# Performance work log

Hardware: AMD Instinct MI355X
Metric: run time of the kernel (lower is better)

Reference implementation:

```python
import jax, jax.numpy as jnp
import numpy as np


def setup_inputs() -> dict:
    key = jax.random.key(0)
    k1, k2 = jax.random.split(key)
    inputs = jax.random.normal(k1, (16, 64, 64, 512), dtype=jnp.float32)
    gamma = jax.random.normal(k2, (1,), dtype=jnp.float32)
    return {"inputs": inputs, "gamma": gamma}


def reference(inputs, gamma):
    # inputs: [B, H, W, C] (NHWC), gamma: [1]
    b, h, w, c = inputs.shape
    vec_a = inputs.reshape(b, h * w, c)           # [B, HW, C]
    # channel-channel Gram matrix: [B, C, C]
    aTa = jnp.einsum('bnc,bnd->bcd', vec_a, vec_a)
    softmax_aTa = jax.nn.softmax(aTa, axis=-1)     # softmax over last channel axis
    # attend over channels: [B, HW, C] @ [B, C, C] -> [B, HW, C]
    aaTa = jnp.einsum('bnc,bcd->bnd', vec_a, softmax_aTa)
    aaTa = aaTa.reshape(b, h, w, c)
    return gamma * aaTa + inputs
```

## Files before the change

kernel.cpp:

```cpp
#include <hip/hip_runtime.h>
#include <stdint.h>

#define BB 16
#define NN 4096
#define CC 512
#define PELEM ((size_t)BB * CC * CC)

typedef __attribute__((ext_vector_type(8))) short bf16x8;
typedef __attribute__((ext_vector_type(4))) float f32x4;

__device__ __forceinline__ unsigned short to_bf16(float f) {
  unsigned int u = __float_as_uint(f);
  u += 0x7fffu + ((u >> 16) & 1u);
  return (unsigned short)(u >> 16);
}
__device__ __forceinline__ float bf16_to_f32(unsigned short h) {
  return __uint_as_float(((unsigned int)h) << 16);
}

__device__ __forceinline__ void gload_lds16(const void* g, void* l) {
  __builtin_amdgcn_global_load_lds(
      (const __attribute__((address_space(1))) unsigned int*)g,
      (__attribute__((address_space(3))) unsigned int*)l, 16, 0, 0);
}

template <int RS, int KLEN>
__device__ __forceinline__ void nt_gemm(const unsigned short* __restrict__ aB,
                                        const unsigned short* __restrict__ bB,
                                        f32x4 acc[4][4],
                                        unsigned short* lds) {
  const int tid  = threadIdx.x;
  const int wid  = tid >> 6;
  const int lane = tid & 63;
  const int wr   = (wid >> 1) * 64;
  const int wc   = (wid & 1) * 64;

  const f32x4 zero = {0.f, 0.f, 0.f, 0.f};
#pragma unroll
  for (int i = 0; i < 4; ++i)
#pragma unroll
    for (int j = 0; j < 4; ++j) acc[i][j] = zero;

  const int srow = lane >> 3;
  const int gsrc = (lane & 7) ^ srow;
  constexpr int NT = KLEN / 64;

  auto stage = [&](int bf, int k0) {
#pragma unroll
    for (int i = 0; i < 4; ++i) {
      const int issue = wid * 4 + i;
      const int row   = issue * 8 + srow;
      const size_t go = (size_t)row * RS + k0 + gsrc * 8;
      gload_lds16(aB + go, lds + bf * 16384 + issue * 512);
      gload_lds16(bB + go, lds + bf * 16384 + 8192 + issue * 512);
    }
  };
  auto compute = [&](int bf) {
    const unsigned short* lA = lds + bf * 16384;
    const unsigned short* lB = lA + 8192;
#pragma unroll
    for (int s = 0; s < 2; ++s) {
      bf16x8 af[4], bfr[4];
#pragma unroll
      for (int mf = 0; mf < 4; ++mf) {
        const int row = wr + mf * 16 + (lane & 15);
        const int ch  = (s * 4 + (lane >> 4)) ^ (row & 7);
        af[mf] = *(const bf16x8*)(lA + row * 64 + ch * 8);
      }
#pragma unroll
      for (int nf = 0; nf < 4; ++nf) {
        const int row = wc + nf * 16 + (lane & 15);
        const int ch  = (s * 4 + (lane >> 4)) ^ (row & 7);
        bfr[nf] = *(const bf16x8*)(lB + row * 64 + ch * 8);
      }
#pragma unroll
      for (int mf = 0; mf < 4; ++mf)
#pragma unroll
        for (int nf = 0; nf < 4; ++nf)
          acc[mf][nf] = __builtin_amdgcn_mfma_f32_16x16x32_bf16(
              af[mf], bfr[nf], acc[mf][nf], 0, 0, 0);
    }
  };

  stage(0, 0);
  __syncthreads();
  int cur = 0;
#pragma unroll 1
  for (int t = 0; t < NT; ++t) {
    if (t + 1 < NT) stage(cur ^ 1, (t + 1) * 64);
    compute(cur);
    __syncthreads();
    cur ^= 1;
  }
}

__global__ __launch_bounds__(256) void k_convert(const float* __restrict__ in,
                                                 unsigned short* __restrict__ a16,
                                                 unsigned short* __restrict__ at16) {
  __shared__ unsigned short lt[64 * 68];
  const int b  = blockIdx.y;
  const int tn = blockIdx.x >> 3, tc = blockIdx.x & 7;
  const int n0 = tn * 64, c0 = tc * 64;
  const int t   = threadIdx.x;
  const int ctc = t & 15;
  const int ntq = t >> 4;

  const float* src = in + ((size_t)b * NN + n0 + 4 * ntq) * CC + c0 + 4 * ctc;
  unsigned short* adst = a16 + ((size_t)b * NN + n0 + 4 * ntq) * CC + c0 + 4 * ctc;

  unsigned short ob[4][4];
#pragma unroll
  for (int j = 0; j < 4; ++j) {
    float4 v = *(const float4*)(src + (size_t)j * CC);
    ob[j][0] = to_bf16(v.x); ob[j][1] = to_bf16(v.y);
    ob[j][2] = to_bf16(v.z); ob[j][3] = to_bf16(v.w);
    ushort4 o = {ob[j][0], ob[j][1], ob[j][2], ob[j][3]};
    *(ushort4*)(adst + (size_t)j * CC) = o;
  }
#pragma unroll
  for (int q = 0; q < 4; ++q) {
    ushort4 w = {ob[0][q], ob[1][q], ob[2][q], ob[3][q]};
    *(ushort4*)&lt[(4 * ctc + q) * 68 + 4 * ntq] = w;
  }
  __syncthreads();

  const int c_l = t >> 2, w4 = t & 3;
  const unsigned short* lr = lt + c_l * 68;
  uint2 r0a = *(const uint2*)(lr + 8 * w4);
  uint2 r0b = *(const uint2*)(lr + 8 * w4 + 4);
  uint2 r1a = *(const uint2*)(lr + 8 * w4 + 32);
  uint2 r1b = *(const uint2*)(lr + 8 * w4 + 36);
  unsigned short* tb = at16 + ((size_t)b * CC + c0 + c_l) * NN + n0;
  uint4 s0 = {r0a.x, r0a.y, r0b.x, r0b.y};
  uint4 s1 = {r1a.x, r1a.y, r1b.x, r1b.y};
  *(uint4*)(tb + 8 * w4)      = s0;
  *(uint4*)(tb + 8 * w4 + 32) = s1;
}

__global__ __launch_bounds__(256) void k_gram(const unsigned short* __restrict__ at,
                                              float* __restrict__ parts) {
  __shared__ __align__(16) unsigned short lds[32768];
  const int bid  = blockIdx.x;
  const int work = (bid & 7) * 80 + (bid >> 3);
  const int b    = work / 40;
  const int r    = work % 40;
  const int ks   = r / 10;
  const int t10  = r % 10;
  const int ti = t10 < 4 ? 0 : t10 < 7 ? 1 : t10 < 9 ? 2 : 3;
  const int tj = t10 < 4 ? t10 : t10 < 7 ? t10 - 3 : t10 < 9 ? t10 - 5 : 3;
  const int c0 = ti * 128, d0 = tj * 128;

  const unsigned short* aB = at + ((size_t)b * CC + c0) * NN + ks * 1024;
  const unsigned short* bB = at + ((size_t)b * CC + d0) * NN + ks * 1024;
  f32x4 acc[4][4];
  nt_gemm<NN, 1024>(aB, bB, acc, lds);

  const int tid = threadIdx.x;
  const int lane = tid & 63, wid = tid >> 6;
  const int wr = (wid >> 1) * 64, wc = (wid & 1) * 64;
  float* gb = parts + (size_t)ks * PELEM + (size_t)b * CC * CC;

#pragma unroll
  for (int mf = 0; mf < 4; ++mf)
#pragma unroll
    for (int nf = 0; nf < 4; ++nf)
#pragma unroll
      for (int q = 0; q < 4; ++q) {
        const int row = c0 + wr + mf * 16 + (lane >> 4) * 4 + q;
        const int col = d0 + wc + nf * 16 + (lane & 15);
        gb[(size_t)row * CC + col] = acc[mf][nf][q];
      }

  if (c0 != d0) {
    float* sf = (float*)lds;
#pragma unroll 1
    for (int h = 0; h < 2; ++h) {
      __syncthreads();
      if ((wid >> 1) == h) {
#pragma unroll
        for (int mf = 0; mf < 4; ++mf)
#pragma unroll
          for (int nf = 0; nf < 4; ++nf)
#pragma unroll
            for (int q = 0; q < 4; ++q) {
              const int row_l = mf * 16 + (lane >> 4) * 4 + q;
              const int col   = wc + nf * 16 + (lane & 15);
              sf[row_l * 132 + col] = acc[mf][nf][q];
            }
      }
      __syncthreads();
      const int d_l = tid >> 1;
      const int rh  = tid & 1;
      float vals[32];
#pragma unroll
      for (int u = 0; u < 32; ++u) vals[u] = sf[(32 * rh + u) * 132 + d_l];
      float* dst = gb + (size_t)(d0 + d_l) * CC + c0 + 64 * h + 32 * rh;
#pragma unroll
      for (int s = 0; s < 8; ++s) {
        float4 w = {vals[4 * s], vals[4 * s + 1], vals[4 * s + 2], vals[4 * s + 3]};
        *(float4*)(dst + 4 * s) = w;
      }
    }
  }
}

__global__ __launch_bounds__(256) void k_softmax(const float* __restrict__ parts,
                                                 unsigned short* __restrict__ st) {
  __shared__ unsigned short ls[32][512];
  const int b  = blockIdx.x >> 4;
  const int cb = blockIdx.x & 15;
  const int wid = threadIdx.x >> 6, lane = threadIdx.x & 63;

#pragma unroll 1
  for (int i = 0; i < 8; ++i) {
    const int rl = wid * 8 + i;
    const int c  = cb * 32 + rl;
    const int r7 = rl & 7;
    const float* base = parts + ((size_t)b * CC + c) * CC;
    float4 v0 = {0.f, 0.f, 0.f, 0.f}, v1 = {0.f, 0.f, 0.f, 0.f};
#pragma unroll
    for (int p = 0; p < 4; ++p) {
      float4 a = *(const float4*)(base + (size_t)p * PELEM + lane * 4);
      float4 bq = *(const float4*)(base + (size_t)p * PELEM + 256 + lane * 4);
      v0.x += a.x; v0.y += a.y; v0.z += a.z; v0.w += a.w;
      v1.x += bq.x; v1.y += bq.y; v1.z += bq.z; v1.w += bq.w;
    }
    float m = fmaxf(fmaxf(fmaxf(v0.x, v0.y), fmaxf(v0.z, v0.w)),
                    fmaxf(fmaxf(v1.x, v1.y), fmaxf(v1.z, v1.w)));
#pragma unroll
    for (int off = 32; off > 0; off >>= 1) m = fmaxf(m, __shfl_xor(m, off));
    float e0 = expf(v0.x - m), e1 = expf(v0.y - m), e2 = expf(v0.z - m), e3 = expf(v0.w - m);
    float e4 = expf(v1.x - m), e5 = expf(v1.y - m), e6 = expf(v1.z - m), e7 = expf(v1.w - m);
    float s = e0 + e1 + e2 + e3 + e4 + e5 + e6 + e7;
#pragma unroll
    for (int off = 32; off > 0; off >>= 1) s += __shfl_xor(s, off);
    const float pinv = 1.0f / s;
    ushort4 o0, o1;
    o0.x = to_bf16(e0 * pinv); o0.y = to_bf16(e1 * pinv);
    o0.z = to_bf16(e2 * pinv); o0.w = to_bf16(e3 * pinv);
    o1.x = to_bf16(e4 * pinv); o1.y = to_bf16(e5 * pinv);
    o1.z = to_bf16(e6 * pinv); o1.w = to_bf16(e7 * pinv);
    *(ushort4*)&ls[rl][(lane ^ r7) << 2]         = o0;
    *(ushort4*)&ls[rl][256 + ((lane ^ r7) << 2)] = o1;
  }
  __syncthreads();

#pragma unroll 1
  for (int i = 0; i < 2; ++i) {
    const int d = i * 256 + threadIdx.x;
    unsigned int u[16];
#pragma unroll
    for (int k = 0; k < 16; ++k) {
      const int c0i = 2 * k, c1i = 2 * k + 1;
      const unsigned int lo = ls[c0i][(((d >> 2) ^ (c0i & 7)) << 2) | (d & 3)];
      const unsigned int hi = ls[c1i][(((d >> 2) ^ (c1i & 7)) << 2) | (d & 3)];
      u[k] = lo | (hi << 16);
    }
    unsigned short* dst = st + ((size_t)b * CC + d) * CC + cb * 32;
    uint4 w0 = {u[0], u[1], u[2], u[3]};
    uint4 w1 = {u[4], u[5], u[6], u[7]};
    uint4 w2 = {u[8], u[9], u[10], u[11]};
    uint4 w3 = {u[12], u[13], u[14], u[15]};
    *(uint4*)(dst + 0)  = w0;
    *(uint4*)(dst + 8)  = w1;
    *(uint4*)(dst + 16) = w2;
    *(uint4*)(dst + 24) = w3;
  }
}

__global__ __launch_bounds__(256) void k_out(const unsigned short* __restrict__ a16,
                                             const unsigned short* __restrict__ st,
                                             const float* __restrict__ gammap,
                                             float* __restrict__ outp) {
  __shared__ __align__(16) unsigned short lds[32768];
  const int bid  = blockIdx.x;
  const int work = (bid & 7) * 256 + (bid >> 3);
  const int b    = work >> 7;
  const int r    = work & 127;
  const int nt   = r >> 5;
  const int mt   = r & 31;
  const int n0 = mt * 128, d0 = nt * 128;
  const unsigned short* aB = a16 + ((size_t)b * NN + n0) * CC;
  const unsigned short* bB = st + ((size_t)b * CC + d0) * CC;
  f32x4 acc[4][4];
  nt_gemm<CC, CC>(aB, bB, acc, lds);

  const float g = gammap[0];
  const int lane = threadIdx.x & 63, wid = threadIdx.x >> 6;
  const int wr = (wid >> 1) * 64, wc = (wid & 1) * 64;
  const unsigned short* xr = a16 + ((size_t)b * NN + n0) * CC + d0;
  float* ob = outp + ((size_t)b * NN + n0) * CC + d0;
#pragma unroll
  for (int mf = 0; mf < 4; ++mf)
#pragma unroll
    for (int nf = 0; nf < 4; ++nf)
#pragma unroll
      for (int q = 0; q < 4; ++q) {
        const int row = wr + mf * 16 + (lane >> 4) * 4 + q;
        const int col = wc + nf * 16 + (lane & 15);
        const size_t off = (size_t)row * CC + col;
        ob[off] = fmaf(g, acc[mf][nf][q], bf16_to_f32(xr[off]));
      }
}

extern "C" void kernel_launch(void* const* d_in, const int* in_sizes, int n_in,
                              void* d_out, int out_size, void* d_ws, size_t ws_size,
                              hipStream_t stream) {
  const float* in    = (const float*)d_in[0];
  const float* gamma = (const float*)d_in[1];
  float* outp = (float*)d_out;

  unsigned short* a16  = (unsigned short*)d_ws;
  unsigned short* stb  = (unsigned short*)((char*)d_ws + ((size_t)64 << 20));
  unsigned short* at16 = (unsigned short*)d_out;
  float*          parts = (float*)((char*)d_out + ((size_t)64 << 20));

  k_convert<<<dim3(512, 16), 256, 0, stream>>>(in, a16, at16);
  k_gram<<<dim3(640), 256, 0, stream>>>(at16, parts);
  k_softmax<<<dim3(256), 256, 0, stream>>>(parts, stb);
  k_out<<<dim3(2048), 256, 0, stream>>>(a16, stb, gamma, outp);
}
```

Before: 356.7 us.

## Enlarge GEMM tiles to 256x256 with 512-thread blocks; compute full Gram

The shared NT-GEMM routine moves from 128x128 tiles with 4 waves to 256x256 tiles with 8 waves. Each wave now holds an 8x4 grid of MFMA accumulators, and the double-buffered LDS staging area grows to 128 KB. The Gram kernel stops using symmetry: it computes all four 256x256 quadrants directly and drops the LDS transpose that mirrored the off-diagonal tiles. The aim is more data reuse per LDS load and fewer, larger blocks. The cost is extra Gram FLOPs, one block per CU with less latency hiding, and higher register pressure.

```diff
diff --git a/kernel.cpp b/kernel.cpp
--- a/kernel.cpp
+++ b/kernel.cpp
@@ -25,19 +25,19 @@
 }
 
 template <int RS, int KLEN>
-__device__ __forceinline__ void nt_gemm(const unsigned short* __restrict__ aB,
-                                        const unsigned short* __restrict__ bB,
-                                        f32x4 acc[4][4],
-                                        unsigned short* lds) {
+__device__ __forceinline__ void nt_gemm256(const unsigned short* __restrict__ aB,
+                                           const unsigned short* __restrict__ bB,
+                                           f32x4 acc[8][4],
+                                           unsigned short* lds) {
   const int tid  = threadIdx.x;
   const int wid  = tid >> 6;
   const int lane = tid & 63;
-  const int wr   = (wid >> 1) * 64;
-  const int wc   = (wid & 1) * 64;
+  const int wr   = (wid >> 2) * 128;
+  const int wc   = (wid & 3) * 64;
 
   const f32x4 zero = {0.f, 0.f, 0.f, 0.f};
 #pragma unroll
-  for (int i = 0; i < 4; ++i)
+  for (int i = 0; i < 8; ++i)
 #pragma unroll
     for (int j = 0; j < 4; ++j) acc[i][j] = zero;
 
@@ -51,18 +51,18 @@
       const int issue = wid * 4 + i;
       const int row   = issue * 8 + srow;
       const size_t go = (size_t)row * RS + k0 + gsrc * 8;
-      gload_lds16(aB + go, lds + bf * 16384 + issue * 512);
-      gload_lds16(bB + go, lds + bf * 16384 + 8192 + issue * 512);
+      gload_lds16(aB + go, lds + bf * 32768 + issue * 512);
+      gload_lds16(bB + go, lds + bf * 32768 + 16384 + issue * 512);
     }
   };
   auto compute = [&](int bf) {
-    const unsigned short* lA = lds + bf * 16384;
-    const unsigned short* lB = lA + 8192;
+    const unsigned short* lA = lds + bf * 32768;
+    const unsigned short* lB = lA + 16384;
 #pragma unroll
     for (int s = 0; s < 2; ++s) {
-      bf16x8 af[4], bfr[4];
-#pragma unroll
-      for (int mf = 0; mf < 4; ++mf) {
+      bf16x8 af[8], bfr[4];
+#pragma unroll
+      for (int mf = 0; mf < 8; ++mf) {
         const int row = wr + mf * 16 + (lane & 15);
         const int ch  = (s * 4 + (lane >> 4)) ^ (row & 7);
         af[mf] = *(const bf16x8*)(lA + row * 64 + ch * 8);
@@ -74,7 +74,7 @@
         bfr[nf] = *(const bf16x8*)(lB + row * 64 + ch * 8);
       }
 #pragma unroll
-      for (int mf = 0; mf < 4; ++mf)
+      for (int mf = 0; mf < 8; ++mf)
 #pragma unroll
         for (int nf = 0; nf < 4; ++nf)
           acc[mf][nf] = __builtin_amdgcn_mfma_f32_16x16x32_bf16(
@@ -137,31 +137,27 @@
   *(uint4*)(tb + 8 * w4 + 32) = s1;
 }
 
-__global__ __launch_bounds__(256) void k_gram(const unsigned short* __restrict__ at,
-                                              float* __restrict__ parts) {
-  __shared__ __align__(16) unsigned short lds[32768];
+__global__ __launch_bounds__(512, 1) void k_gram(const unsigned short* __restrict__ at,
+                                                 float* __restrict__ parts) {
+  __shared__ __align__(16) unsigned short lds[65536];
   const int bid  = blockIdx.x;
-  const int work = (bid & 7) * 80 + (bid >> 3);
-  const int b    = work / 40;
-  const int r    = work % 40;
-  const int ks   = r / 10;
-  const int t10  = r % 10;
-  const int ti = t10 < 4 ? 0 : t10 < 7 ? 1 : t10 < 9 ? 2 : 3;
-  const int tj = t10 < 4 ? t10 : t10 < 7 ? t10 - 3 : t10 < 9 ? t10 - 5 : 3;
-  const int c0 = ti * 128, d0 = tj * 128;
-
+  const int work = (bid & 7) * 32 + (bid >> 3);
+  const int b    = work >> 4;
+  const int r    = work & 15;
+  const int ks   = r >> 2;
+  const int tile = r & 3;
+  const int c0 = (tile & 1) * 256;
+  const int d0 = (tile >> 1) * 256;
   const unsigned short* aB = at + ((size_t)b * CC + c0) * NN + ks * 1024;
   const unsigned short* bB = at + ((size_t)b * CC + d0) * NN + ks * 1024;
-  f32x4 acc[4][4];
-  nt_gemm<NN, 1024>(aB, bB, acc, lds);
-
-  const int tid = threadIdx.x;
-  const int lane = tid & 63, wid = tid >> 6;
-  const int wr = (wid >> 1) * 64, wc = (wid & 1) * 64;
+  f32x4 acc[8][4];
+  nt_gemm256<NN, 1024>(aB, bB, acc, lds);
+
+  const int lane = threadIdx.x & 63, wid = threadIdx.x >> 6;
+  const int wr = (wid >> 2) * 128, wc = (wid & 3) * 64;
   float* gb = parts + (size_t)ks * PELEM + (size_t)b * CC * CC;
-
-#pragma unroll
-  for (int mf = 0; mf < 4; ++mf)
+#pragma unroll
+  for (int mf = 0; mf < 8; ++mf)
 #pragma unroll
     for (int nf = 0; nf < 4; ++nf)
 #pragma unroll
@@ -170,38 +166,6 @@
         const int col = d0 + wc + nf * 16 + (lane & 15);
         gb[(size_t)row * CC + col] = acc[mf][nf][q];
       }
-
-  if (c0 != d0) {
-    float* sf = (float*)lds;
-#pragma unroll 1
-    for (int h = 0; h < 2; ++h) {
-      __syncthreads();
-      if ((wid >> 1) == h) {
-#pragma unroll
-        for (int mf = 0; mf < 4; ++mf)
-#pragma unroll
-          for (int nf = 0; nf < 4; ++nf)
-#pragma unroll
-            for (int q = 0; q < 4; ++q) {
-              const int row_l = mf * 16 + (lane >> 4) * 4 + q;
-              const int col   = wc + nf * 16 + (lane & 15);
-              sf[row_l * 132 + col] = acc[mf][nf][q];
-            }
-      }
-      __syncthreads();
-      const int d_l = tid >> 1;
-      const int rh  = tid & 1;
-      float vals[32];
-#pragma unroll
-      for (int u = 0; u < 32; ++u) vals[u] = sf[(32 * rh + u) * 132 + d_l];
-      float* dst = gb + (size_t)(d0 + d_l) * CC + c0 + 64 * h + 32 * rh;
-#pragma unroll
-      for (int s = 0; s < 8; ++s) {
-        float4 w = {vals[4 * s], vals[4 * s + 1], vals[4 * s + 2], vals[4 * s + 3]};
-        *(float4*)(dst + 4 * s) = w;
-      }
-    }
-  }
 }
 
 __global__ __launch_bounds__(256) void k_softmax(const float* __restrict__ parts,
@@ -268,30 +232,30 @@
   }
 }
 
-__global__ __launch_bounds__(256) void k_out(const unsigned short* __restrict__ a16,
-                                             const unsigned short* __restrict__ st,
-                                             const float* __restrict__ gammap,
-                                             float* __restrict__ outp) {
-  __shared__ __align__(16) unsigned short lds[32768];
+__global__ __launch_bounds__(512, 1) void k_out(const unsigned short* __restrict__ a16,
+                                                const unsigned short* __restrict__ st,
+                                                const float* __restrict__ gammap,
+                                                float* __restrict__ outp) {
+  __shared__ __align__(16) unsigned short lds[65536];
   const int bid  = blockIdx.x;
-  const int work = (bid & 7) * 256 + (bid >> 3);
-  const int b    = work >> 7;
-  const int r    = work & 127;
-  const int nt   = r >> 5;
-  const int mt   = r & 31;
-  const int n0 = mt * 128, d0 = nt * 128;
+  const int work = (bid & 7) * 64 + (bid >> 3);
+  const int b    = work >> 5;
+  const int r    = work & 31;
+  const int nt   = r >> 4;
+  const int mt   = r & 15;
+  const int n0 = mt * 256, d0 = nt * 256;
   const unsigned short* aB = a16 + ((size_t)b * NN + n0) * CC;
   const unsigned short* bB = st + ((size_t)b * CC + d0) * CC;
-  f32x4 acc[4][4];
-  nt_gemm<CC, CC>(aB, bB, acc, lds);
+  f32x4 acc[8][4];
+  nt_gemm256<CC, CC>(aB, bB, acc, lds);
 
   const float g = gammap[0];
   const int lane = threadIdx.x & 63, wid = threadIdx.x >> 6;
-  const int wr = (wid >> 1) * 64, wc = (wid & 1) * 64;
+  const int wr = (wid >> 2) * 128, wc = (wid & 3) * 64;
   const unsigned short* xr = a16 + ((size_t)b * NN + n0) * CC + d0;
   float* ob = outp + ((size_t)b * NN + n0) * CC + d0;
 #pragma unroll
-  for (int mf = 0; mf < 4; ++mf)
+  for (int mf = 0; mf < 8; ++mf)
 #pragma unroll
     for (int nf = 0; nf < 4; ++nf)
 #pragma unroll
@@ -316,7 +280,7 @@
   float*          parts = (float*)((char*)d_out + ((size_t)64 << 20));
 
   k_convert<<<dim3(512, 16), 256, 0, stream>>>(in, a16, at16);
-  k_gram<<<dim3(640), 256, 0, stream>>>(at16, parts);
+  k_gram<<<dim3(256), 512, 0, stream>>>(at16, parts);
   k_softmax<<<dim3(256), 256, 0, stream>>>(parts, stb);
-  k_out<<<dim3(2048), 256, 0, stream>>>(a16, stb, gamma, outp);
-}
+  k_out<<<dim3(512), 512, 0, stream>>>(a16, stb, gamma, outp);
+}
```

New measurement: 352.6 us. Within noise of the previous version (-1.1%).
